# Kernel optimization log

Hardware: AMD Instinct MI355X
Metric: run time of the kernel (lower is better)

Reference implementation:

```python
import jax, jax.numpy as jnp
import numpy as np

# FP4 lookup table (E2M1-style values) exactly as in FP4Codec.FP4_TABLE
FP4_TABLE = jnp.array([0.0, 0.5, 1.0, 1.5, 2.0, 3.0, 4.0, 6.0,
                       0.0, -0.5, -1.0, -1.5, -2.0, -3.0, -4.0, -6.0],
                      dtype=jnp.float32)

M, K, N = 128, 4096, 16384


def setup_inputs() -> dict:
    key = jax.random.key(0)
    k1, k2, k3, k4 = jax.random.split(key, 4)
    x = jax.random.normal(k1, (M, K), dtype=jnp.float32)
    # packed bytes: each int holds two 4-bit FP4 indices (hi<<4 | lo)
    weight_fp4 = jax.random.randint(k2, (N, K // 2), 0, 256, dtype=jnp.int32)
    # positive per-output-channel scale (encode guarantees >= 1e-8)
    weight_scale = jax.random.uniform(k3, (N,), dtype=jnp.float32,
                                      minval=1e-3, maxval=2e-2)
    bias = jax.random.normal(k4, (N,), dtype=jnp.float32) * 0.02
    return {"x": x, "weight_fp4": weight_fp4,
            "weight_scale": weight_scale, "bias": bias}


def _dequantize(weight_fp4, weight_scale):
    p = weight_fp4.astype(jnp.uint8)
    hi = (p >> 4) & 0xF
    lo = p & 0xF
    # interleave [hi, lo] along last dim -> [N, K] indices
    idx = jnp.stack([hi, lo], axis=-1).reshape(p.shape[0], -1)
    return FP4_TABLE[idx] * weight_scale[:, None]  # [N, K] fp32


def reference(x, weight_fp4, weight_scale, bias):
    w = _dequantize(weight_fp4, weight_scale)          # [N, K]
    y = jnp.einsum('mk,nk->mn', x, w) + bias            # [M, N]
    return jax.nn.gelu(y, approximate=False)            # exact GELU like F.gelu
```

## Files before the change

### kernel.cpp

```cpp
#include <hip/hip_runtime.h>
#include <stdint.h>


#define M_DIM 128
#define K_DIM 4096
#define N_DIM 16384
#define BN    64
#define BK    64
#define NK    (K_DIM/BK)
#define NT    512
#define NBLK  (N_DIM/BN)

#define A_BYTES 16384
#define B_BYTES 8192
#define NBUF    4
#define AOFF(b) ((b)*A_BYTES)
#define BOFF(b) (NBUF*A_BYTES + (b)*B_BYTES)
#define LDS_SZ  (NBUF*(A_BYTES+B_BYTES))

typedef __attribute__((ext_vector_type(8))) __bf16 bf16x8;
typedef __attribute__((ext_vector_type(4))) float  f32x4;
typedef unsigned short ushort_t;

__device__ __forceinline__ unsigned f2b_bits(float f) {
  unsigned u = __builtin_bit_cast(unsigned, f);
  u += 0x7FFFu + ((u >> 16) & 1u);
  return u >> 16;
}

__global__ void convert_x_kernel(const float* __restrict__ x,
                                 ushort_t* __restrict__ xb) {
  int i = (blockIdx.x * blockDim.x + threadIdx.x) * 4;
  float4 v = *(const float4*)(x + i);
  ushort4 p;
  p.x = (ushort_t)f2b_bits(v.x);
  p.y = (ushort_t)f2b_bits(v.y);
  p.z = (ushort_t)f2b_bits(v.z);
  p.w = (ushort_t)f2b_bits(v.w);
  *(ushort4*)(xb + i) = p;
}

__device__ __forceinline__ void gl16(const void* g, void* l) {
  __builtin_amdgcn_global_load_lds(
      (const __attribute__((address_space(1))) void*)g,
      (__attribute__((address_space(3))) void*)l, 16, 0, 0);
}

__device__ __forceinline__ bf16x8 decode8(uint4 p) {
  unsigned u01 = __builtin_amdgcn_perm(p.y, p.x, 0x04000400u);
  unsigned u23 = __builtin_amdgcn_perm(p.w, p.z, 0x04000400u);
  unsigned q   = __builtin_amdgcn_perm(u23, u01, 0x05040100u);
  unsigned e  = (q >> 4) & 0x0F0F0F0Fu;
  unsigned o  = q & 0x0F0F0F0Fu;
  unsigned em = e & 0x07070707u, om = o & 0x07070707u;
  unsigned elo = __builtin_amdgcn_perm(0xC0804000u, 0xC0800000u, em);
  unsigned ehi = __builtin_amdgcn_perm(0x40404040u, 0x3F3F3F00u, em);
  unsigned olo = __builtin_amdgcn_perm(0xC0804000u, 0xC0800000u, om);
  unsigned ohi = __builtin_amdgcn_perm(0x40404040u, 0x3F3F3F00u, om);
  ehi |= (e & 0x08080808u) << 4;
  ohi |= (o & 0x08080808u) << 4;
  unsigned t0 = __builtin_amdgcn_perm(ehi, elo, 0x05010400u);
  unsigned t1 = __builtin_amdgcn_perm(ohi, olo, 0x05010400u);
  unsigned t2 = __builtin_amdgcn_perm(ehi, elo, 0x07030602u);
  unsigned t3 = __builtin_amdgcn_perm(ohi, olo, 0x07030602u);
  uint4 r;
  r.x = __builtin_amdgcn_perm(t1, t0, 0x05040100u);
  r.y = __builtin_amdgcn_perm(t1, t0, 0x07060302u);
  r.z = __builtin_amdgcn_perm(t3, t2, 0x05040100u);
  r.w = __builtin_amdgcn_perm(t3, t2, 0x07060302u);
  return __builtin_bit_cast(bf16x8, r);
}

#define MFMA16(a_, b_, c_) __builtin_amdgcn_mfma_f32_16x16x32_bf16(a_, b_, c_, 0, 0, 0)

template<bool USE_XB>
__global__ __launch_bounds__(NT) void fp4gemm_kernel(
    const void* __restrict__ xsrc,
    const int*  __restrict__ wq,
    const float* __restrict__ scale,
    const float* __restrict__ bias,
    float* __restrict__ out) {
  __shared__ __align__(16) uint8_t lds[LDS_SZ];

  const int t   = threadIdx.x;
  const int w   = t >> 6;
  const int l   = t & 63;
  const int l16 = l & 15;
  const int lq  = l >> 4;
  const int mq  = w >> 1;
  const int nh  = w & 1;

  const int bid = blockIdx.x;
  const int n0  = ((bid & 7) * (NBLK / 8) + (bid >> 3)) * BN;

  const int srow = t >> 3;
  const int scol = (t & 7) * 16;
  const int sswz = (srow & 7) << 4;
  const int scbs = scol ^ sswz;
  const int bwr  = srow * 128 + (scol ^ sswz);

  const uint8_t* xb  = (const uint8_t*)xsrc;
  const uint8_t* wqb = (const uint8_t*)wq;

  uint4 rs0, rs1, rs2, rs3;

#define ISSUE_A(k_, b_) do { \
  gl16(xb + (size_t)(srow) * 8192 + (size_t)(k_) * 128 + scbs, \
       lds + AOFF(b_) + w * 1024); \
  gl16(xb + (size_t)(64 + srow) * 8192 + (size_t)(k_) * 128 + scbs, \
       lds + AOFF(b_) + 8192 + w * 1024); \
} while (0)

#define ISSUE_B(k_, s_) do { \
  rs##s_ = *(const uint4*)(wqb + (size_t)(n0 + srow) * 8192 + (size_t)(k_) * 128 + scol); \
} while (0)

#define DECODE_B(s_, b_) do { \
  *(bf16x8*)(lds + BOFF(b_) + bwr) = decode8(rs##s_); \
} while (0)

#define WAITV(N_) asm volatile("s_waitcnt vmcnt(" #N_ ")" ::: "memory")
#define BARRIER() do { \
  asm volatile("s_waitcnt lgkmcnt(0)" ::: "memory"); \
  __builtin_amdgcn_s_barrier(); \
  __builtin_amdgcn_sched_barrier(0); \
} while (0)

  f32x4 acc00 = {0,0,0,0}, acc01 = {0,0,0,0};
  f32x4 acc10 = {0,0,0,0}, acc11 = {0,0,0,0};

  const int cBase = (lq << 4) ^ ((l16 & 7) << 4);
  const int aR0 = (mq * 32 + l16) * 128;
  const int bR0 = (nh * 32 + l16) * 128;

#define COMPUTE(b_) do { \
  const uint8_t* Ab_ = lds + AOFF(b_); \
  const uint8_t* Bb_ = lds + BOFF(b_); \
  _Pragma("unroll") \
  for (int ks_ = 0; ks_ < 2; ++ks_) { \
    const int cS_ = (ks_ << 6) ^ cBase; \
    bf16x8 a0_ = *(const bf16x8*)(Ab_ + aR0 + cS_); \
    bf16x8 a1_ = *(const bf16x8*)(Ab_ + aR0 + 2048 + cS_); \
    bf16x8 b0_ = *(const bf16x8*)(Bb_ + bR0 + cS_); \
    bf16x8 b1_ = *(const bf16x8*)(Bb_ + bR0 + 2048 + cS_); \
    acc00 = MFMA16(a0_, b0_, acc00); \
    acc01 = MFMA16(a0_, b1_, acc01); \
    acc10 = MFMA16(a1_, b0_, acc10); \
    acc11 = MFMA16(a1_, b1_, acc11); \
  } \
} while (0)

#define BODY(k_, u_, cb_) do { \
  ISSUE_A((k_) + 2, u_); \
  WAITV(6); \
  BARRIER(); \
  DECODE_B(u_, u_); \
  ISSUE_B((k_) + 6, u_); \
  COMPUTE(cb_); \
} while (0)

  if constexpr (USE_XB) {
    ISSUE_B(0, 0); ISSUE_B(1, 1); ISSUE_B(2, 2); ISSUE_B(3, 3);
    ISSUE_A(0, 0); ISSUE_A(1, 1);
    WAITV(4);
    DECODE_B(0, 0); DECODE_B(1, 1);
    ISSUE_B(4, 0); ISSUE_B(5, 1);
    ISSUE_A(2, 2); WAITV(6); BARRIER();
    DECODE_B(2, 2); ISSUE_B(6, 2); COMPUTE(0);
    ISSUE_A(3, 3); WAITV(7); BARRIER();
    DECODE_B(3, 3); ISSUE_B(7, 3); COMPUTE(1);
    for (int j = 0; j < 14; ++j) {
      const int kt = 2 + 4 * j;
      BODY(kt + 0, 0, 2);
      BODY(kt + 1, 1, 3);
      BODY(kt + 2, 2, 0);
      BODY(kt + 3, 3, 1);
    }
    ISSUE_A(60, 0); WAITV(6); BARRIER(); DECODE_B(0, 0); COMPUTE(2);
    ISSUE_A(61, 1); WAITV(5); BARRIER(); DECODE_B(1, 1); COMPUTE(3);
    ISSUE_A(62, 2); WAITV(4); BARRIER(); DECODE_B(2, 2); COMPUTE(0);
    ISSUE_A(63, 3); WAITV(4); BARRIER(); DECODE_B(3, 3); COMPUTE(1);
    WAITV(2); BARRIER(); COMPUTE(2);
    WAITV(0); BARRIER(); COMPUTE(3);
  } else {
    for (int kt = 0; kt < NK; ++kt) {
      __syncthreads();
#pragma unroll
      for (int i = 0; i < 2; ++i) {
        const float* xf = (const float*)xsrc +
            (size_t)(i * 64 + srow) * K_DIM + (size_t)kt * BK + (scol >> 1);
        float4 v0 = *(const float4*)(xf);
        float4 v1 = *(const float4*)(xf + 4);
        uint4 pk = make_uint4(f2b_bits(v0.x) | (f2b_bits(v0.y) << 16),
                              f2b_bits(v0.z) | (f2b_bits(v0.w) << 16),
                              f2b_bits(v1.x) | (f2b_bits(v1.y) << 16),
                              f2b_bits(v1.z) | (f2b_bits(v1.w) << 16));
        *(uint4*)(lds + AOFF(kt & 1) + (size_t)(i * 64 + srow) * 128 +
                  (scol ^ sswz)) = pk;
      }
      {
        uint4 pv = *(const uint4*)(wqb + (size_t)(n0 + srow) * 8192 +
                                   (size_t)kt * 128 + scol);
        *(bf16x8*)(lds + BOFF(kt & 1) + bwr) = decode8(pv);
      }
      __syncthreads();
      COMPUTE(kt & 1);
    }
  }

  const int ng = n0 + nh * 32 + l16;
#pragma unroll
  for (int ni = 0; ni < 2; ++ni) {
    const int ngc = ng + ni * 16;
    const float s  = scale[ngc];
    const float bb = bias[ngc];
    f32x4 v0 = ni ? acc01 : acc00;
    f32x4 v1 = ni ? acc11 : acc10;
#pragma unroll
    for (int mi = 0; mi < 2; ++mi) {
      f32x4 vv = mi ? v1 : v0;
#pragma unroll
      for (int j = 0; j < 4; ++j) {
        int m = mq * 32 + mi * 16 + lq * 4 + j;
        float y = vv[j] * s + bb;
        float g = 0.5f * y * (1.0f + erff(y * 0.70710678118654752f));
        out[(size_t)m * N_DIM + ngc] = g;
      }
    }
  }
#undef ISSUE_A
#undef ISSUE_B
#undef DECODE_B
#undef WAITV
#undef BARRIER
#undef COMPUTE
#undef BODY
}

extern "C" void kernel_launch(void* const* d_in, const int* in_sizes, int n_in,
                              void* d_out, int out_size, void* d_ws, size_t ws_size,
                              hipStream_t stream) {
  const float* x     = (const float*)d_in[0];
  const int*   wq    = (const int*)d_in[1];
  const float* scale = (const float*)d_in[2];
  const float* bias  = (const float*)d_in[3];
  float* out = (float*)d_out;

  const size_t xb_bytes = (size_t)M_DIM * K_DIM * sizeof(ushort_t);
  if (ws_size >= xb_bytes) {
    ushort_t* xb = (ushort_t*)d_ws;
    convert_x_kernel<<<(M_DIM * K_DIM) / (256 * 4), 256, 0, stream>>>(x, xb);
    fp4gemm_kernel<true><<<NBLK, NT, 0, stream>>>(xb, wq, scale, bias, out);
  } else {
    fp4gemm_kernel<false><<<NBLK, NT, 0, stream>>>(x, wq, scale, bias, out);
  }
}
```

Baseline: 42.14 us.

## Split K in two across blocks and add a separate reduce+GELU kernel

Each 64-column output tile is now computed by two blocks, each covering half of K, which doubles the grid from 256 to 512 blocks. Each block writes fp32 partial sums to workspace. A new elementwise kernel adds the two partials and applies scale, bias and exact GELU. The LDS staging ring shrinks to three buffers, decoupled from the four register slots, so more blocks can be resident per CU. The aim is to raise occupancy and latency hiding in this weight-streaming, bandwidth-bound GEMM, at the cost of about 16 MB of extra partial-sum traffic, one more kernel launch, and a larger workspace requirement.

```diff
diff --git a/kernel.cpp b/kernel.cpp
--- a/kernel.cpp
+++ b/kernel.cpp
@@ -5,18 +5,18 @@
 #define M_DIM 128
 #define K_DIM 4096
 #define N_DIM 16384
-#define BN    64
 #define BK    64
-#define NK    (K_DIM/BK)
+#define KTH   32
 #define NT    512
-#define NBLK  (N_DIM/BN)
-
-#define A_BYTES 16384
-#define B_BYTES 8192
-#define NBUF    4
-#define AOFF(b) ((b)*A_BYTES)
-#define BOFF(b) (NBUF*A_BYTES + (b)*B_BYTES)
-#define LDS_SZ  (NBUF*(A_BYTES+B_BYTES))
+#define NBLK_G 512
+
+#define A3OFF(i) ((i)*16384)
+#define B3OFF(i) (49152 + (i)*8192)
+#define LDS_SZ   73728
+
+#define XB_BYTES ((size_t)M_DIM*K_DIM*2)
+#define MN       ((size_t)M_DIM*N_DIM)
+#define PART_BYTES (2*MN*4)
 
 typedef __attribute__((ext_vector_type(8))) __bf16 bf16x8;
 typedef __attribute__((ext_vector_type(4))) float  f32x4;
@@ -28,8 +28,8 @@
   return u >> 16;
 }
 
-__global__ void convert_x_kernel(const float* __restrict__ x,
-                                 ushort_t* __restrict__ xb) {
+__global__ __launch_bounds__(256) void convert_x_kernel(
+    const float* __restrict__ x, ushort_t* __restrict__ xb) {
   int i = (blockIdx.x * blockDim.x + threadIdx.x) * 4;
   float4 v = *(const float4*)(x + i);
   ushort4 p;
@@ -73,13 +73,10 @@
 
 #define MFMA16(a_, b_, c_) __builtin_amdgcn_mfma_f32_16x16x32_bf16(a_, b_, c_, 0, 0, 0)
 
-template<bool USE_XB>
-__global__ __launch_bounds__(NT) void fp4gemm_kernel(
-    const void* __restrict__ xsrc,
+__global__ __launch_bounds__(NT, 4) void fp4gemm_split_kernel(
+    const ushort_t* __restrict__ xsrc,
     const int*  __restrict__ wq,
-    const float* __restrict__ scale,
-    const float* __restrict__ bias,
-    float* __restrict__ out) {
+    float* __restrict__ partial) {
   __shared__ __align__(16) uint8_t lds[LDS_SZ];
 
   const int t   = threadIdx.x;
@@ -90,8 +87,10 @@
   const int mq  = w >> 1;
   const int nh  = w & 1;
 
-  const int bid = blockIdx.x;
-  const int n0  = ((bid & 7) * (NBLK / 8) + (bid >> 3)) * BN;
+  const int bid   = blockIdx.x;
+  const int n0    = ((bid & 7) * 32 + (bid >> 4)) * 64;
+  const int khalf = (bid >> 3) & 1;
+  const int kgB   = khalf * KTH;
 
   const int srow = t >> 3;
   const int scol = (t & 7) * 16;
@@ -102,21 +101,22 @@
   const uint8_t* xb  = (const uint8_t*)xsrc;
   const uint8_t* wqb = (const uint8_t*)wq;
 
-  uint4 rs0, rs1, rs2, rs3;
-
-#define ISSUE_A(k_, b_) do { \
-  gl16(xb + (size_t)(srow) * 8192 + (size_t)(k_) * 128 + scbs, \
-       lds + AOFF(b_) + w * 1024); \
-  gl16(xb + (size_t)(64 + srow) * 8192 + (size_t)(k_) * 128 + scbs, \
-       lds + AOFF(b_) + 8192 + w * 1024); \
+  uint4 rq0, rq1, rq2, rq3;
+
+#define ISSUE_A(k_, u3_) do { \
+  gl16(xb + (size_t)(srow) * 8192 + (size_t)(kgB + (k_)) * 128 + scbs, \
+       lds + A3OFF(u3_) + w * 1024); \
+  gl16(xb + (size_t)(64 + srow) * 8192 + (size_t)(kgB + (k_)) * 128 + scbs, \
+       lds + A3OFF(u3_) + 8192 + w * 1024); \
 } while (0)
 
 #define ISSUE_B(k_, s_) do { \
-  rs##s_ = *(const uint4*)(wqb + (size_t)(n0 + srow) * 8192 + (size_t)(k_) * 128 + scol); \
-} while (0)
-
-#define DECODE_B(s_, b_) do { \
-  *(bf16x8*)(lds + BOFF(b_) + bwr) = decode8(rs##s_); \
+  rq##s_ = *(const uint4*)(wqb + (size_t)(n0 + srow) * 8192 + \
+                           (size_t)(kgB + (k_)) * 128 + scol); \
+} while (0)
+
+#define DECODE_B(s_, u3_) do { \
+  *(bf16x8*)(lds + B3OFF(u3_) + bwr) = decode8(rq##s_); \
 } while (0)
 
 #define WAITV(N_) asm volatile("s_waitcnt vmcnt(" #N_ ")" ::: "memory")
@@ -129,16 +129,16 @@
   f32x4 acc00 = {0,0,0,0}, acc01 = {0,0,0,0};
   f32x4 acc10 = {0,0,0,0}, acc11 = {0,0,0,0};
 
-  const int cBase = (lq << 4) ^ ((l16 & 7) << 4);
   const int aR0 = (mq * 32 + l16) * 128;
   const int bR0 = (nh * 32 + l16) * 128;
-
-#define COMPUTE(b_) do { \
-  const uint8_t* Ab_ = lds + AOFF(b_); \
-  const uint8_t* Bb_ = lds + BOFF(b_); \
+  const int cB  = (lq << 4) ^ ((l16 & 7) << 4);
+
+#define COMPUTE(c3_) do { \
+  const uint8_t* Ab_ = lds + A3OFF(c3_); \
+  const uint8_t* Bb_ = lds + B3OFF(c3_); \
   _Pragma("unroll") \
   for (int ks_ = 0; ks_ < 2; ++ks_) { \
-    const int cS_ = (ks_ << 6) ^ cBase; \
+    const int cS_ = (ks_ << 6) ^ cB; \
     bf16x8 a0_ = *(const bf16x8*)(Ab_ + aR0 + cS_); \
     bf16x8 a1_ = *(const bf16x8*)(Ab_ + aR0 + 2048 + cS_); \
     bf16x8 b0_ = *(const bf16x8*)(Bb_ + bR0 + cS_); \
@@ -150,81 +150,53 @@
   } \
 } while (0)
 
-#define BODY(k_, u_, cb_) do { \
-  ISSUE_A((k_) + 2, u_); \
-  WAITV(6); \
+#define BODY_S(k_, s4_, u3_, c3_) do { \
+  WAITV(3); \
   BARRIER(); \
-  DECODE_B(u_, u_); \
-  ISSUE_B((k_) + 6, u_); \
-  COMPUTE(cb_); \
-} while (0)
-
-  if constexpr (USE_XB) {
-    ISSUE_B(0, 0); ISSUE_B(1, 1); ISSUE_B(2, 2); ISSUE_B(3, 3);
-    ISSUE_A(0, 0); ISSUE_A(1, 1);
-    WAITV(4);
-    DECODE_B(0, 0); DECODE_B(1, 1);
-    ISSUE_B(4, 0); ISSUE_B(5, 1);
-    ISSUE_A(2, 2); WAITV(6); BARRIER();
-    DECODE_B(2, 2); ISSUE_B(6, 2); COMPUTE(0);
-    ISSUE_A(3, 3); WAITV(7); BARRIER();
-    DECODE_B(3, 3); ISSUE_B(7, 3); COMPUTE(1);
-    for (int j = 0; j < 14; ++j) {
-      const int kt = 2 + 4 * j;
-      BODY(kt + 0, 0, 2);
-      BODY(kt + 1, 1, 3);
-      BODY(kt + 2, 2, 0);
-      BODY(kt + 3, 3, 1);
-    }
-    ISSUE_A(60, 0); WAITV(6); BARRIER(); DECODE_B(0, 0); COMPUTE(2);
-    ISSUE_A(61, 1); WAITV(5); BARRIER(); DECODE_B(1, 1); COMPUTE(3);
-    ISSUE_A(62, 2); WAITV(4); BARRIER(); DECODE_B(2, 2); COMPUTE(0);
-    ISSUE_A(63, 3); WAITV(4); BARRIER(); DECODE_B(3, 3); COMPUTE(1);
-    WAITV(2); BARRIER(); COMPUTE(2);
-    WAITV(0); BARRIER(); COMPUTE(3);
-  } else {
-    for (int kt = 0; kt < NK; ++kt) {
-      __syncthreads();
-#pragma unroll
-      for (int i = 0; i < 2; ++i) {
-        const float* xf = (const float*)xsrc +
-            (size_t)(i * 64 + srow) * K_DIM + (size_t)kt * BK + (scol >> 1);
-        float4 v0 = *(const float4*)(xf);
-        float4 v1 = *(const float4*)(xf + 4);
-        uint4 pk = make_uint4(f2b_bits(v0.x) | (f2b_bits(v0.y) << 16),
-                              f2b_bits(v0.z) | (f2b_bits(v0.w) << 16),
-                              f2b_bits(v1.x) | (f2b_bits(v1.y) << 16),
-                              f2b_bits(v1.z) | (f2b_bits(v1.w) << 16));
-        *(uint4*)(lds + AOFF(kt & 1) + (size_t)(i * 64 + srow) * 128 +
-                  (scol ^ sswz)) = pk;
-      }
-      {
-        uint4 pv = *(const uint4*)(wqb + (size_t)(n0 + srow) * 8192 +
-                                   (size_t)kt * 128 + scol);
-        *(bf16x8*)(lds + BOFF(kt & 1) + bwr) = decode8(pv);
-      }
-      __syncthreads();
-      COMPUTE(kt & 1);
-    }
-  }
-
-  const int ng = n0 + nh * 32 + l16;
-#pragma unroll
-  for (int ni = 0; ni < 2; ++ni) {
-    const int ngc = ng + ni * 16;
-    const float s  = scale[ngc];
-    const float bb = bias[ngc];
-    f32x4 v0 = ni ? acc01 : acc00;
-    f32x4 v1 = ni ? acc11 : acc10;
-#pragma unroll
-    for (int mi = 0; mi < 2; ++mi) {
-      f32x4 vv = mi ? v1 : v0;
+  DECODE_B(s4_, u3_); \
+  ISSUE_B((k_) + 6, s4_); \
+  ISSUE_A((k_) + 2, u3_); \
+  COMPUTE(c3_); \
+} while (0)
+
+#define GROUP12(k0_) do { \
+  BODY_S((k0_)+0, 0,1,2); BODY_S((k0_)+1, 1,2,0); BODY_S((k0_)+2, 2,0,1); \
+  BODY_S((k0_)+3, 3,1,2); BODY_S((k0_)+4, 0,2,0); BODY_S((k0_)+5, 1,0,1); \
+  BODY_S((k0_)+6, 2,1,2); BODY_S((k0_)+7, 3,2,0); BODY_S((k0_)+8, 0,0,1); \
+  BODY_S((k0_)+9, 1,1,2); BODY_S((k0_)+10,2,2,0); BODY_S((k0_)+11,3,0,1); \
+} while (0)
+
+  ISSUE_B(0, 0); ISSUE_B(1, 1); ISSUE_B(2, 2); ISSUE_B(3, 3);
+  ISSUE_A(0, 0); ISSUE_A(1, 1);
+  WAITV(4);
+  DECODE_B(0, 0); DECODE_B(1, 1);
+  ISSUE_B(4, 0); ISSUE_B(5, 1);
+  WAITV(4); BARRIER();
+  DECODE_B(2, 2); ISSUE_B(6, 2); ISSUE_A(2, 2); COMPUTE(0);
+  WAITV(5); BARRIER();
+  DECODE_B(3, 0); ISSUE_B(7, 3); ISSUE_A(3, 0); COMPUTE(1);
+  GROUP12(2);
+  GROUP12(14);
+  WAITV(3); BARRIER(); DECODE_B(0, 1); ISSUE_A(28, 1); COMPUTE(2);
+  WAITV(2); BARRIER(); DECODE_B(1, 2); ISSUE_A(29, 2); COMPUTE(0);
+  WAITV(2); BARRIER(); DECODE_B(2, 0); ISSUE_A(30, 0); COMPUTE(1);
+  WAITV(2); BARRIER(); DECODE_B(3, 1); ISSUE_A(31, 1); COMPUTE(2);
+  WAITV(2); BARRIER(); COMPUTE(0);
+  WAITV(0); BARRIER(); COMPUTE(1);
+
+  float* pk = partial + (size_t)khalf * MN;
+#pragma unroll
+  for (int c = 0; c < 2; ++c) {
+    const int ngc = n0 + nh * 32 + c * 16 + l16;
+    f32x4 v0 = c ? acc01 : acc00;
+    f32x4 v1 = c ? acc11 : acc10;
+#pragma unroll
+    for (int fr = 0; fr < 2; ++fr) {
+      f32x4 vv = fr ? v1 : v0;
 #pragma unroll
       for (int j = 0; j < 4; ++j) {
-        int m = mq * 32 + mi * 16 + lq * 4 + j;
-        float y = vv[j] * s + bb;
-        float g = 0.5f * y * (1.0f + erff(y * 0.70710678118654752f));
-        out[(size_t)m * N_DIM + ngc] = g;
+        int m = mq * 32 + fr * 16 + lq * 4 + j;
+        pk[(size_t)m * N_DIM + ngc] = vv[j];
       }
     }
   }
@@ -234,7 +206,103 @@
 #undef WAITV
 #undef BARRIER
 #undef COMPUTE
-#undef BODY
+#undef BODY_S
+#undef GROUP12
+}
+
+__global__ __launch_bounds__(256) void reduce_gelu_kernel(
+    const float* __restrict__ partial,
+    const float* __restrict__ scale,
+    const float* __restrict__ bias,
+    float* __restrict__ out) {
+  size_t idx = ((size_t)blockIdx.x * 256 + threadIdx.x) * 4;
+  float4 a = *(const float4*)(partial + idx);
+  float4 b = *(const float4*)(partial + MN + idx);
+  int n = (int)(idx & (N_DIM - 1));
+  float4 s  = *(const float4*)(scale + n);
+  float4 bb = *(const float4*)(bias + n);
+  float4 r;
+  {
+    float y;
+    y = (a.x + b.x) * s.x + bb.x; r.x = 0.5f * y * (1.0f + erff(y * 0.70710678118654752f));
+    y = (a.y + b.y) * s.y + bb.y; r.y = 0.5f * y * (1.0f + erff(y * 0.70710678118654752f));
+    y = (a.z + b.z) * s.z + bb.z; r.z = 0.5f * y * (1.0f + erff(y * 0.70710678118654752f));
+    y = (a.w + b.w) * s.w + bb.w; r.w = 0.5f * y * (1.0f + erff(y * 0.70710678118654752f));
+  }
+  *(float4*)(out + idx) = r;
+}
+
+__global__ __launch_bounds__(NT) void fp4gemm_fallback_kernel(
+    const float* __restrict__ x, const int* __restrict__ wq,
+    const float* __restrict__ scale, const float* __restrict__ bias,
+    float* __restrict__ out) {
+  __shared__ __align__(16) uint8_t lds[LDS_SZ];
+  const int t = threadIdx.x, w = t >> 6, l = t & 63;
+  const int l16 = l & 15, lq = l >> 4, mq = w >> 1, nh = w & 1;
+  const int n0 = (int)blockIdx.x * 64;
+  const int srow = t >> 3, scol = (t & 7) * 16, sswz = (srow & 7) << 4;
+  const int bwr = srow * 128 + (scol ^ sswz);
+  const uint8_t* wqb = (const uint8_t*)wq;
+  f32x4 acc00 = {0,0,0,0}, acc01 = {0,0,0,0};
+  f32x4 acc10 = {0,0,0,0}, acc11 = {0,0,0,0};
+  const int aR0 = (mq * 32 + l16) * 128;
+  const int bR0 = (nh * 32 + l16) * 128;
+  const int cB  = (lq << 4) ^ ((l16 & 7) << 4);
+  for (int kt = 0; kt < 64; ++kt) {
+    __syncthreads();
+    int bb = kt & 1;
+#pragma unroll
+    for (int i = 0; i < 2; ++i) {
+      const float* xf = x + (size_t)(i * 64 + srow) * K_DIM + (size_t)kt * BK + (scol >> 1);
+      float4 v0 = *(const float4*)(xf);
+      float4 v1 = *(const float4*)(xf + 4);
+      uint4 pk = make_uint4(f2b_bits(v0.x) | (f2b_bits(v0.y) << 16),
+                            f2b_bits(v0.z) | (f2b_bits(v0.w) << 16),
+                            f2b_bits(v1.x) | (f2b_bits(v1.y) << 16),
+                            f2b_bits(v1.z) | (f2b_bits(v1.w) << 16));
+      *(uint4*)(lds + A3OFF(bb) + (size_t)(i * 64 + srow) * 128 + (scol ^ sswz)) = pk;
+    }
+    {
+      uint4 pv = *(const uint4*)(wqb + (size_t)(n0 + srow) * 8192 + (size_t)kt * 128 + scol);
+      *(bf16x8*)(lds + B3OFF(bb) + bwr) = decode8(pv);
+    }
+    __syncthreads();
+    {
+      const uint8_t* Ab_ = lds + A3OFF(bb);
+      const uint8_t* Bb_ = lds + B3OFF(bb);
+#pragma unroll
+      for (int ks = 0; ks < 2; ++ks) {
+        const int cS = (ks << 6) ^ cB;
+        bf16x8 a0 = *(const bf16x8*)(Ab_ + aR0 + cS);
+        bf16x8 a1 = *(const bf16x8*)(Ab_ + aR0 + 2048 + cS);
+        bf16x8 b0 = *(const bf16x8*)(Bb_ + bR0 + cS);
+        bf16x8 b1 = *(const bf16x8*)(Bb_ + bR0 + 2048 + cS);
+        acc00 = MFMA16(a0, b0, acc00);
+        acc01 = MFMA16(a0, b1, acc01);
+        acc10 = MFMA16(a1, b0, acc10);
+        acc11 = MFMA16(a1, b1, acc11);
+      }
+    }
+  }
+#pragma unroll
+  for (int c = 0; c < 2; ++c) {
+    const int ngc = n0 + nh * 32 + c * 16 + l16;
+    const float s = scale[ngc];
+    const float bv = bias[ngc];
+    f32x4 v0 = c ? acc01 : acc00;
+    f32x4 v1 = c ? acc11 : acc10;
+#pragma unroll
+    for (int fr = 0; fr < 2; ++fr) {
+      f32x4 vv = fr ? v1 : v0;
+#pragma unroll
+      for (int j = 0; j < 4; ++j) {
+        int m = mq * 32 + fr * 16 + lq * 4 + j;
+        float y = vv[j] * s + bv;
+        out[(size_t)m * N_DIM + ngc] =
+            0.5f * y * (1.0f + erff(y * 0.70710678118654752f));
+      }
+    }
+  }
 }
 
 extern "C" void kernel_launch(void* const* d_in, const int* in_sizes, int n_in,
@@ -246,12 +314,15 @@
   const float* bias  = (const float*)d_in[3];
   float* out = (float*)d_out;
 
-  const size_t xb_bytes = (size_t)M_DIM * K_DIM * sizeof(ushort_t);
-  if (ws_size >= xb_bytes) {
+  if (ws_size >= XB_BYTES + PART_BYTES) {
     ushort_t* xb = (ushort_t*)d_ws;
+    float* partial = (float*)((uint8_t*)d_ws + XB_BYTES);
     convert_x_kernel<<<(M_DIM * K_DIM) / (256 * 4), 256, 0, stream>>>(x, xb);
-    fp4gemm_kernel<true><<<NBLK, NT, 0, stream>>>(xb, wq, scale, bias, out);
+    fp4gemm_split_kernel<<<NBLK_G, NT, 0, stream>>>(xb, wq, partial);
+    reduce_gelu_kernel<<<(int)(MN / (256 * 4)), 256, 0, stream>>>(
+        partial, scale, bias, out);
   } else {
-    fp4gemm_kernel<false><<<NBLK, NT, 0, stream>>>(x, wq, scale, bias, out);
-  }
-}
+    fp4gemm_fallback_kernel<<<N_DIM / 64, NT, 0, stream>>>(
+        x, wq, scale, bias, out);
+  }
+}
```

Measured after the change: 43.26 us. +2.7%, slower.
